# Kernel tuning notes

Hardware: AMD Instinct MI355X
Metric: run time of the kernel (lower is better)

The kernel has to match this reference:

```python
import jax, jax.numpy as jnp
import numpy as np

N_LEVELS = 8
N_FEATS = 8            # features per level
BASE_RES = 16
PER_LEVEL_SCALE = 1.2599210739135742
LOG2_HASHMAP = 19
TABLE_PAD = 8192       # padded per-level table rows (>= max level size 6568)
N_POINTS = 262144


def _level_params(l):
    # tcnn: scale = base * s^l - 1 ; res = ceil(scale)+1 ; size = min(2^19, round_up(res^2, 8))
    scale = BASE_RES * (PER_LEVEL_SCALE ** l) - 1.0
    res = int(np.ceil(scale)) + 1
    size = min(1 << LOG2_HASHMAP, ((res * res + 7) // 8) * 8)
    return float(scale), res, size


def hashgrid_encode(x, table):
    """x: [N,2] in [0,1), table: [L, TABLE_PAD, F]. Returns [N, L*F]."""
    outs = []
    for l in range(N_LEVELS):
        scale, res, size = _level_params(l)
        pos = x * jnp.float32(scale) + jnp.float32(0.5)
        pg = jnp.floor(pos)
        frac = pos - pg
        pg = pg.astype(jnp.int32)
        # Smoothstep interpolation weights: t^2 (3 - 2t)
        w = frac * frac * (3.0 - 2.0 * frac)          # [N,2]
        feat = jnp.zeros((x.shape[0], N_FEATS), dtype=table.dtype)
        for dx in (0, 1):
            wx = w[:, 0] if dx else 1.0 - w[:, 0]
            for dy in (0, 1):
                wy = w[:, 1] if dy else 1.0 - w[:, 1]
                # dense grid index (all levels here fit the hashmap), modulo level size as in tcnn
                idx = ((pg[:, 0] + dx) + (pg[:, 1] + dy) * res) % size
                feat = feat + (wx * wy)[:, None] * table[l, idx]  # irregular gather
        outs.append(feat)
    return jnp.concatenate(outs, axis=-1)  # [N, 64]


def mlp(enc, W0, W1, W2, W3):
    h = jax.nn.relu(enc @ W0)
    h = jax.nn.relu(h @ W1)
    h = jax.nn.relu(h @ W2)
    return h @ W3  # linear output activation


def setup_inputs() -> dict:
    key = jax.random.key(0)
    ks = jax.random.split(key, 6)
    x = jax.random.uniform(ks[0], (N_POINTS, 2), dtype=jnp.float32)
    # tcnn initializes grid params ~ uniform(-1e-4, 1e-4); small values
    table = jax.random.normal(ks[1], (N_LEVELS, TABLE_PAD, N_FEATS), dtype=jnp.float32) * 1e-2
    W0 = jax.random.normal(ks[2], (64, 256), dtype=jnp.float32) * (1.0 / np.sqrt(64))
    W1 = jax.random.normal(ks[3], (256, 256), dtype=jnp.float32) * (1.0 / np.sqrt(256))
    W2 = jax.random.normal(ks[4], (256, 256), dtype=jnp.float32) * (1.0 / np.sqrt(256))
    W3 = jax.random.normal(ks[5], (256, 1), dtype=jnp.float32) * (1.0 / np.sqrt(256))
    return {"x": x, "table": table, "W0": W0, "W1": W1, "W2": W2, "W3": W3}


def reference(x, table, W0, W1, W2, W3):
    enc = hashgrid_encode(x, table)
    return mlp(enc, W0, W1, W2, W3)  # [N, 1]
```

## Files before the change

kernel.cpp:

```cpp
#include <hip/hip_runtime.h>
#include <cmath>


#define N_LEVELS 8
#define TABLE_PAD 8192
#define TILE_M 64
#define ACT_STRIDE 264
#define ENC_STRIDE 72

typedef __attribute__((ext_vector_type(8))) short short8;
typedef __attribute__((ext_vector_type(16))) float float16v;

struct LevelParams {
  float scale[N_LEVELS];
  int   res[N_LEVELS];
  int   size[N_LEVELS];
};

__device__ __forceinline__ unsigned short f2bf(float f) {
  unsigned int u = __float_as_uint(f);
  u += 0x7fffu + ((u >> 16) & 1u);
  return (unsigned short)(u >> 16);
}
__device__ __forceinline__ unsigned int pack2bf(float a, float b) {
  a = a > 0.f ? a : 0.f;
  b = b > 0.f ? b : 0.f;
  return (unsigned int)f2bf(a) | ((unsigned int)f2bf(b) << 16);
}

__global__ void pack_weights_kernel(const float* __restrict__ W0,
                                    const float* __restrict__ W1,
                                    const float* __restrict__ W2,
                                    unsigned short* __restrict__ Wp) {
  int tid = blockIdx.x * blockDim.x + threadIdx.x;
  const float* src;
  int base, e;
  if (tid < 16384)        { src = W0; base = 0;     e = tid;         }
  else if (tid < 81920)   { src = W1; base = 16384; e = tid - 16384; }
  else if (tid < 147456)  { src = W2; base = 81920; e = tid - 81920; }
  else return;
  int ki = e & 15;
  int n  = (e >> 4) & 255;
  int kb = e >> 12;
  unsigned int u = __float_as_uint(src[(kb * 16 + ki) * 256 + n]);
  u += 0x7fffu + ((u >> 16) & 1u);
  Wp[base + e] = (unsigned short)(u >> 16);
}

__global__ __launch_bounds__(512, 6) void neural_field_kernel(
    const float* __restrict__ x,
    const float* __restrict__ table,
    const unsigned short* __restrict__ Wp,
    const float* __restrict__ W3,
    float* __restrict__ out,
    LevelParams P) {
  __shared__ unsigned short bufE[TILE_M * ENC_STRIDE];
  __shared__ unsigned short bufA[TILE_M * ACT_STRIDE];

  const int t  = threadIdx.x;
  const int g0 = blockIdx.x * TILE_M;

  const int lane  = t & 63;
  const int w     = t >> 6;
  const int l31   = lane & 31;
  const int h8    = lane >> 5;
  const int wbase = w * 32;

  const int woff = (wbase + l31) * 16 + h8 * 8;

  {
    int p = t & 63;
    int l = t >> 6;
    float2 xy = ((const float2*)x)[g0 + p];
    float scale = P.scale[l];
    int res = P.res[l], size = P.size[l];
    float posx = xy.x * scale + 0.5f;
    float posy = xy.y * scale + 0.5f;
    float pgx = floorf(posx), pgy = floorf(posy);
    float fx = posx - pgx, fy = posy - pgy;
    float wx = fx * fx * (3.0f - 2.0f * fx);
    float wy = fy * fy * (3.0f - 2.0f * fy);
    int px = (int)pgx, py = (int)pgy;
    float acc[8] = {0, 0, 0, 0, 0, 0, 0, 0};
    for (int dy = 0; dy < 2; ++dy) {
      float wyv = dy ? wy : 1.0f - wy;
      for (int dx = 0; dx < 2; ++dx) {
        float wgt = (dx ? wx : 1.0f - wx) * wyv;
        int idx = (px + dx) + (py + dy) * res;
        if (idx >= size) idx -= size;
        const float4* tp =
            (const float4*)(table + ((size_t)l * TABLE_PAD + idx) * 8);
        float4 t0 = tp[0], t1 = tp[1];
        acc[0] += wgt * t0.x; acc[1] += wgt * t0.y;
        acc[2] += wgt * t0.z; acc[3] += wgt * t0.w;
        acc[4] += wgt * t1.x; acc[5] += wgt * t1.y;
        acc[6] += wgt * t1.z; acc[7] += wgt * t1.w;
      }
    }
    union { unsigned short s[8]; short8 v; } u;
    for (int j = 0; j < 8; ++j) u.s[j] = f2bf(acc[j]);
    *(short8*)&bufE[p * ENC_STRIDE + l * 8] = u.v;
  }

  auto run_layer = [&](const unsigned short* inb, int in_stride,
                       unsigned short* outb, const unsigned short* Wpl,
                       int KB, short8 wf0, bool inplace, bool fuse_final,
                       float* fsum) {
    float16v acc[2];
    for (int j = 0; j < 16; ++j) { acc[0][j] = 0.f; acc[1][j] = 0.f; }

    const unsigned short* ap0 = &inb[l31 * in_stride + h8 * 8];
    const unsigned short* ap1 = ap0 + 32 * in_stride;
    const unsigned short* wp  = Wpl + woff;

    float w3f[16];
    if (fuse_final) {
      for (int q = 0; q < 4; ++q) {
        float4 wv = *(const float4*)(W3 + wbase + 8 * q + 4 * h8);
        w3f[4 * q + 0] = wv.x; w3f[4 * q + 1] = wv.y;
        w3f[4 * q + 2] = wv.z; w3f[4 * q + 3] = wv.w;
      }
    }

    short8 af0[2];
    af0[0] = *(const short8*)(ap0);
    af0[1] = *(const short8*)(ap1);

#pragma unroll
    for (int kb = 0; kb < KB; ++kb) {
      short8 wf1, af1[2];
      int kn = (kb + 1 < KB) ? kb + 1 : kb;
      wf1    = *(const short8*)(wp + kn * 4096);
      af1[0] = *(const short8*)(ap0 + kn * 16);
      af1[1] = *(const short8*)(ap1 + kn * 16);

      acc[0] = __builtin_amdgcn_mfma_f32_32x32x16_bf16(wf0, af0[0], acc[0],
                                                       0, 0, 0);
      acc[1] = __builtin_amdgcn_mfma_f32_32x32x16_bf16(wf0, af0[1], acc[1],
                                                       0, 0, 0);
      wf0 = wf1; af0[0] = af1[0]; af0[1] = af1[1];
    }

    if (inplace) __syncthreads();

    if (!fuse_final) {
      for (int pt = 0; pt < 2; ++pt) {
        int m = pt * 32 + l31;
        for (int q = 0; q < 4; ++q) {
          int n0 = wbase + 8 * q + 4 * h8;
          uint2 pk;
          pk.x = pack2bf(acc[pt][4 * q + 0], acc[pt][4 * q + 1]);
          pk.y = pack2bf(acc[pt][4 * q + 2], acc[pt][4 * q + 3]);
          *(uint2*)&outb[m * ACT_STRIDE + n0] = pk;
        }
      }
    } else {
      float part0 = 0.f, part1 = 0.f;
      for (int j = 0; j < 16; ++j) {
        float v0 = acc[0][j]; v0 = v0 > 0.f ? v0 : 0.f;
        float v1 = acc[1][j]; v1 = v1 > 0.f ? v1 : 0.f;
        part0 += v0 * w3f[j];
        part1 += v1 * w3f[j];
      }
      part0 += __shfl_xor(part0, 32);
      part1 += __shfl_xor(part1, 32);
      float val = h8 ? part1 : part0;
      fsum[lane * 9 + w] = val;
    }
  };

  float* fsum = (float*)bufE;

  short8 wf = *(const short8*)(Wp + woff);
  __syncthreads();
  run_layer(bufE, ENC_STRIDE, bufA, Wp, 4, wf, false, false, fsum);
  wf = *(const short8*)(Wp + 16384 + woff);
  __syncthreads();
  run_layer(bufA, ACT_STRIDE, bufA, Wp + 16384, 16, wf, true, false, fsum);
  wf = *(const short8*)(Wp + 81920 + woff);
  __syncthreads();
  run_layer(bufA, ACT_STRIDE, nullptr, Wp + 81920, 16, wf, false, true, fsum);
  __syncthreads();

  {
    int p = t >> 3;
    int q = t & 7;
    float v = fsum[p * 9 + q];
    v += __shfl_xor(v, 1);
    v += __shfl_xor(v, 2);
    v += __shfl_xor(v, 4);
    if (q == 0) out[g0 + p] = v;
  }
}

extern "C" void kernel_launch(void* const* d_in, const int* in_sizes, int n_in,
                              void* d_out, int out_size, void* d_ws,
                              size_t ws_size, hipStream_t stream) {
  const float* x     = (const float*)d_in[0];
  const float* table = (const float*)d_in[1];
  const float* W0    = (const float*)d_in[2];
  const float* W1    = (const float*)d_in[3];
  const float* W2    = (const float*)d_in[4];
  const float* W3    = (const float*)d_in[5];
  float* out = (float*)d_out;
  int N = in_sizes[0] / 2;

  unsigned short* Wp = (unsigned short*)d_ws;

  LevelParams P;
  const double c = 1.2599210739135742;
  double m = 1.0;
  for (int l = 0; l < N_LEVELS; ++l) {
    double scale_d = 16.0 * m - 1.0;
    int res = (int)std::ceil(scale_d) + 1;
    long long sz = ((long long)res * res + 7) / 8 * 8;
    if (sz > (1LL << 19)) sz = 1LL << 19;
    P.scale[l] = (float)scale_d;
    P.res[l]   = res;
    P.size[l]  = (int)sz;
    m *= c;
  }

  hipLaunchKernelGGL(pack_weights_kernel, dim3(576), dim3(256), 0, stream,
                     W0, W1, W2, Wp);
  hipLaunchKernelGGL(neural_field_kernel, dim3(N / TILE_M), dim3(512), 0,
                     stream, x, table, Wp, W3, out, P);
}
```

Baseline: 156.2 us.

## Enlarge point tile to 96 rows with three MFMA row-tiles per wave

```diff
diff --git a/kernel.cpp b/kernel.cpp
--- a/kernel.cpp
+++ b/kernel.cpp
@@ -4,7 +4,7 @@
 
 #define N_LEVELS 8
 #define TABLE_PAD 8192
-#define TILE_M 64
+#define TILE_M 96
 #define ACT_STRIDE 264
 #define ENC_STRIDE 72
 
@@ -47,13 +47,13 @@
   Wp[base + e] = (unsigned short)(u >> 16);
 }
 
-__global__ __launch_bounds__(512, 6) void neural_field_kernel(
+__global__ __launch_bounds__(512, 4) void neural_field_kernel(
     const float* __restrict__ x,
     const float* __restrict__ table,
     const unsigned short* __restrict__ Wp,
     const float* __restrict__ W3,
     float* __restrict__ out,
-    LevelParams P) {
+    LevelParams P, int Ntot) {
   __shared__ unsigned short bufE[TILE_M * ENC_STRIDE];
   __shared__ unsigned short bufA[TILE_M * ACT_STRIDE];
 
@@ -69,103 +69,115 @@
   const int woff = (wbase + l31) * 16 + h8 * 8;
 
   {
-    int p = t & 63;
-    int l = t >> 6;
-    float2 xy = ((const float2*)x)[g0 + p];
-    float scale = P.scale[l];
-    int res = P.res[l], size = P.size[l];
-    float posx = xy.x * scale + 0.5f;
-    float posy = xy.y * scale + 0.5f;
-    float pgx = floorf(posx), pgy = floorf(posy);
-    float fx = posx - pgx, fy = posy - pgy;
-    float wx = fx * fx * (3.0f - 2.0f * fx);
-    float wy = fy * fy * (3.0f - 2.0f * fy);
-    int px = (int)pgx, py = (int)pgy;
-    float acc[8] = {0, 0, 0, 0, 0, 0, 0, 0};
-    for (int dy = 0; dy < 2; ++dy) {
-      float wyv = dy ? wy : 1.0f - wy;
-      for (int dx = 0; dx < 2; ++dx) {
-        float wgt = (dx ? wx : 1.0f - wx) * wyv;
-        int idx = (px + dx) + (py + dy) * res;
-        if (idx >= size) idx -= size;
-        const float4* tp =
-            (const float4*)(table + ((size_t)l * TABLE_PAD + idx) * 8);
-        float4 t0 = tp[0], t1 = tp[1];
-        acc[0] += wgt * t0.x; acc[1] += wgt * t0.y;
-        acc[2] += wgt * t0.z; acc[3] += wgt * t0.w;
-        acc[4] += wgt * t1.x; acc[5] += wgt * t1.y;
-        acc[6] += wgt * t1.z; acc[7] += wgt * t1.w;
-      }
-    }
-    union { unsigned short s[8]; short8 v; } u;
-    for (int j = 0; j < 8; ++j) u.s[j] = f2bf(acc[j]);
-    *(short8*)&bufE[p * ENC_STRIDE + l * 8] = u.v;
+    int p  = t & 127;
+    int lg = t >> 7;
+    if (p < TILE_M) {
+      int gi = g0 + p;
+      if (gi >= Ntot) gi = Ntot - 1;
+      float2 xy = ((const float2*)x)[gi];
+      for (int li = 0; li < 2; ++li) {
+        int l = lg * 2 + li;
+        float scale = P.scale[l];
+        int res = P.res[l], size = P.size[l];
+        float posx = xy.x * scale + 0.5f;
+        float posy = xy.y * scale + 0.5f;
+        float pgx = floorf(posx), pgy = floorf(posy);
+        float fx = posx - pgx, fy = posy - pgy;
+        float wx = fx * fx * (3.0f - 2.0f * fx);
+        float wy = fy * fy * (3.0f - 2.0f * fy);
+        int px = (int)pgx, py = (int)pgy;
+        float acc[8] = {0, 0, 0, 0, 0, 0, 0, 0};
+        for (int dy = 0; dy < 2; ++dy) {
+          float wyv = dy ? wy : 1.0f - wy;
+          for (int dx = 0; dx < 2; ++dx) {
+            float wgt = (dx ? wx : 1.0f - wx) * wyv;
+            int idx = (px + dx) + (py + dy) * res;
+            if (idx >= size) idx -= size;
+            const float4* tp =
+                (const float4*)(table + ((size_t)l * TABLE_PAD + idx) * 8);
+            float4 t0 = tp[0], t1 = tp[1];
+            acc[0] += wgt * t0.x; acc[1] += wgt * t0.y;
+            acc[2] += wgt * t0.z; acc[3] += wgt * t0.w;
+            acc[4] += wgt * t1.x; acc[5] += wgt * t1.y;
+            acc[6] += wgt * t1.z; acc[7] += wgt * t1.w;
+          }
+        }
+        union { unsigned short s[8]; short8 v; } u;
+        for (int j = 0; j < 8; ++j) u.s[j] = f2bf(acc[j]);
+        *(short8*)&bufE[p * ENC_STRIDE + l * 8] = u.v;
+      }
+    }
   }
 
   auto run_layer = [&](const unsigned short* inb, int in_stride,
                        unsigned short* outb, const unsigned short* Wpl,
                        int KB, short8 wf0, bool inplace, bool fuse_final,
                        float* fsum) {
-    float16v acc[2];
-    for (int j = 0; j < 16; ++j) { acc[0][j] = 0.f; acc[1][j] = 0.f; }
-
-    const unsigned short* ap0 = &inb[l31 * in_stride + h8 * 8];
-    const unsigned short* ap1 = ap0 + 32 * in_stride;
-    const unsigned short* wp  = Wpl + woff;
-
-    float w3f[16];
-    if (fuse_final) {
-      for (int q = 0; q < 4; ++q) {
-        float4 wv = *(const float4*)(W3 + wbase + 8 * q + 4 * h8);
-        w3f[4 * q + 0] = wv.x; w3f[4 * q + 1] = wv.y;
-        w3f[4 * q + 2] = wv.z; w3f[4 * q + 3] = wv.w;
-      }
-    }
-
-    short8 af0[2];
-    af0[0] = *(const short8*)(ap0);
-    af0[1] = *(const short8*)(ap1);
+    float16v acc[3];
+    for (int pt = 0; pt < 3; ++pt)
+      for (int j = 0; j < 16; ++j) acc[pt][j] = 0.f;
+
+    const unsigned short* ap[3];
+    for (int pt = 0; pt < 3; ++pt)
+      ap[pt] = &inb[(pt * 32 + l31) * in_stride + h8 * 8];
+    const unsigned short* wp = Wpl + woff;
+
+    short8 af0[3];
+    for (int pt = 0; pt < 3; ++pt)
+      af0[pt] = *(const short8*)(ap[pt]);
 
 #pragma unroll
     for (int kb = 0; kb < KB; ++kb) {
-      short8 wf1, af1[2];
       int kn = (kb + 1 < KB) ? kb + 1 : kb;
-      wf1    = *(const short8*)(wp + kn * 4096);
-      af1[0] = *(const short8*)(ap0 + kn * 16);
-      af1[1] = *(const short8*)(ap1 + kn * 16);
-
-      acc[0] = __builtin_amdgcn_mfma_f32_32x32x16_bf16(wf0, af0[0], acc[0],
-                                                       0, 0, 0);
-      acc[1] = __builtin_amdgcn_mfma_f32_32x32x16_bf16(wf0, af0[1], acc[1],
-                                                       0, 0, 0);
-      wf0 = wf1; af0[0] = af1[0]; af0[1] = af1[1];
+      short8 wf1 = *(const short8*)(wp + kn * 4096);
+      short8 af1[3];
+      for (int pt = 0; pt < 3; ++pt)
+        af1[pt] = *(const short8*)(ap[pt] + kn * 16);
+
+      for (int pt = 0; pt < 3; ++pt)
+        acc[pt] = __builtin_amdgcn_mfma_f32_32x32x16_bf16(wf0, af0[pt],
+                                                          acc[pt], 0, 0, 0);
+      wf0 = wf1;
+      for (int pt = 0; pt < 3; ++pt) af0[pt] = af1[pt];
     }
 
     if (inplace) __syncthreads();
 
     if (!fuse_final) {
-      for (int pt = 0; pt < 2; ++pt) {
+      for (int pt = 0; pt < 3; ++pt) {
         int m = pt * 32 + l31;
         for (int q = 0; q < 4; ++q) {
           int n0 = wbase + 8 * q + 4 * h8;
           uint2 pk;
           pk.x = pack2bf(acc[pt][4 * q + 0], acc[pt][4 * q + 1]);
           pk.y = pack2bf(acc[pt][4 * q + 2], acc[pt][4 * q + 3]);
-          *(uint2*)&outb[m * ACT_STRIDE + n0] = pk;
+          *(uint2*)&bufA[m * ACT_STRIDE + n0] = pk;
         }
       }
     } else {
-      float part0 = 0.f, part1 = 0.f;
-      for (int j = 0; j < 16; ++j) {
-        float v0 = acc[0][j]; v0 = v0 > 0.f ? v0 : 0.f;
-        float v1 = acc[1][j]; v1 = v1 > 0.f ? v1 : 0.f;
-        part0 += v0 * w3f[j];
-        part1 += v1 * w3f[j];
-      }
-      part0 += __shfl_xor(part0, 32);
-      part1 += __shfl_xor(part1, 32);
-      float val = h8 ? part1 : part0;
-      fsum[lane * 9 + w] = val;
+      float w3f[16];
+      for (int q = 0; q < 4; ++q) {
+        float4 wv = *(const float4*)(W3 + wbase + 8 * q + 4 * h8);
+        w3f[4 * q + 0] = wv.x; w3f[4 * q + 1] = wv.y;
+        w3f[4 * q + 2] = wv.z; w3f[4 * q + 3] = wv.w;
+      }
+      float part[3];
+      for (int pt = 0; pt < 3; ++pt) {
+        float s = 0.f;
+        for (int j = 0; j < 16; ++j) {
+          float v = acc[pt][j]; v = v > 0.f ? v : 0.f;
+          s += v * w3f[j];
+        }
+        part[pt] = s;
+      }
+      for (int pt = 0; pt < 3; ++pt)
+        part[pt] += __shfl_xor(part[pt], 32);
+      if (h8 == 0) {
+        fsum[(l31)      * 9 + w] = part[0];
+        fsum[(32 + l31) * 9 + w] = part[1];
+      } else {
+        fsum[(64 + l31) * 9 + w] = part[2];
+      }
     }
   };
 
@@ -183,13 +195,15 @@
   __syncthreads();
 
   {
-    int p = t >> 3;
-    int q = t & 7;
-    float v = fsum[p * 9 + q];
+    int p = t >> 2;
+    int q = t & 3;
+    float v = fsum[p * 9 + q] + fsum[p * 9 + q + 4];
     v += __shfl_xor(v, 1);
     v += __shfl_xor(v, 2);
-    v += __shfl_xor(v, 4);
-    if (q == 0) out[g0 + p] = v;
+    if (q == 0 && p < TILE_M) {
+      int gi = g0 + p;
+      if (gi < Ntot) out[gi] = v;
+    }
   }
 }
 
@@ -221,8 +235,9 @@
     m *= c;
   }
 
+  int nblocks = (N + TILE_M - 1) / TILE_M;
   hipLaunchKernelGGL(pack_weights_kernel, dim3(576), dim3(256), 0, stream,
                      W0, W1, W2, Wp);
-  hipLaunchKernelGGL(neural_field_kernel, dim3(N / TILE_M), dim3(512), 0,
-                     stream, x, table, Wp, W3, out, P);
-}
+  hipLaunchKernelGGL(neural_field_kernel, dim3(nblocks), dim3(512), 0,
+                     stream, x, table, Wp, W3, out, P, N);
+}
```

Result: no change. 156.9 us (+0.5%).

## Remap MFMA wave tiling to 64 features by 32 points per wave

Applied to the files above, without the earlier changes.

```diff
diff --git a/kernel.cpp b/kernel.cpp
--- a/kernel.cpp
+++ b/kernel.cpp
@@ -1,4 +1,5 @@
 #include <hip/hip_runtime.h>
+#include <hip/hip_bf16.h>
 #include <cmath>
 
 
@@ -22,10 +23,11 @@
   u += 0x7fffu + ((u >> 16) & 1u);
   return (unsigned short)(u >> 16);
 }
-__device__ __forceinline__ unsigned int pack2bf(float a, float b) {
+__device__ __forceinline__ unsigned int pack2bf_relu(float a, float b) {
   a = a > 0.f ? a : 0.f;
   b = b > 0.f ? b : 0.f;
-  return (unsigned int)f2bf(a) | ((unsigned int)f2bf(b) << 16);
+  __hip_bfloat162 h = __float22bfloat162_rn(make_float2(a, b));
+  return *(unsigned int*)&h;
 }
 
 __global__ void pack_weights_kernel(const float* __restrict__ W0,
@@ -64,9 +66,12 @@
   const int w     = t >> 6;
   const int l31   = lane & 31;
   const int h8    = lane >> 5;
-  const int wbase = w * 32;
-
-  const int woff = (wbase + l31) * 16 + h8 * 8;
+  const int fgrp  = w & 3;
+  const int pgrp  = w >> 2;
+  const int fbase = fgrp * 64;
+  const int mrow  = pgrp * 32 + l31;
+
+  const int woff = (fbase + l31) * 16 + h8 * 8;
 
   {
     int p = t & 63;
@@ -103,92 +108,70 @@
   }
 
   auto run_layer = [&](const unsigned short* inb, int in_stride,
-                       unsigned short* outb, const unsigned short* Wpl,
-                       int KB, short8 wf0, bool inplace, bool fuse_final,
-                       float* fsum) {
+                       const unsigned short* Wpl, int KB,
+                       bool inplace, bool fuse_final, float* fsum) {
     float16v acc[2];
     for (int j = 0; j < 16; ++j) { acc[0][j] = 0.f; acc[1][j] = 0.f; }
 
-    const unsigned short* ap0 = &inb[l31 * in_stride + h8 * 8];
-    const unsigned short* ap1 = ap0 + 32 * in_stride;
-    const unsigned short* wp  = Wpl + woff;
-
-    float w3f[16];
-    if (fuse_final) {
-      for (int q = 0; q < 4; ++q) {
-        float4 wv = *(const float4*)(W3 + wbase + 8 * q + 4 * h8);
-        w3f[4 * q + 0] = wv.x; w3f[4 * q + 1] = wv.y;
-        w3f[4 * q + 2] = wv.z; w3f[4 * q + 3] = wv.w;
-      }
-    }
-
-    short8 af0[2];
-    af0[0] = *(const short8*)(ap0);
-    af0[1] = *(const short8*)(ap1);
+    const unsigned short* ap = &inb[mrow * in_stride + h8 * 8];
+    const unsigned short* wp = Wpl + woff;
 
 #pragma unroll
     for (int kb = 0; kb < KB; ++kb) {
-      short8 wf1, af1[2];
-      int kn = (kb + 1 < KB) ? kb + 1 : kb;
-      wf1    = *(const short8*)(wp + kn * 4096);
-      af1[0] = *(const short8*)(ap0 + kn * 16);
-      af1[1] = *(const short8*)(ap1 + kn * 16);
-
-      acc[0] = __builtin_amdgcn_mfma_f32_32x32x16_bf16(wf0, af0[0], acc[0],
+      short8 wf0 = *(const short8*)(wp + kb * 4096);
+      short8 wf1 = *(const short8*)(wp + kb * 4096 + 512);
+      short8 af  = *(const short8*)(ap + kb * 16);
+      acc[0] = __builtin_amdgcn_mfma_f32_32x32x16_bf16(wf0, af, acc[0],
                                                        0, 0, 0);
-      acc[1] = __builtin_amdgcn_mfma_f32_32x32x16_bf16(wf0, af0[1], acc[1],
+      acc[1] = __builtin_amdgcn_mfma_f32_32x32x16_bf16(wf1, af, acc[1],
                                                        0, 0, 0);
-      wf0 = wf1; af0[0] = af1[0]; af0[1] = af1[1];
     }
 
     if (inplace) __syncthreads();
 
     if (!fuse_final) {
-      for (int pt = 0; pt < 2; ++pt) {
-        int m = pt * 32 + l31;
+      for (int f2 = 0; f2 < 2; ++f2) {
         for (int q = 0; q < 4; ++q) {
-          int n0 = wbase + 8 * q + 4 * h8;
+          int n0 = fbase + f2 * 32 + 8 * q + 4 * h8;
           uint2 pk;
-          pk.x = pack2bf(acc[pt][4 * q + 0], acc[pt][4 * q + 1]);
-          pk.y = pack2bf(acc[pt][4 * q + 2], acc[pt][4 * q + 3]);
-          *(uint2*)&outb[m * ACT_STRIDE + n0] = pk;
+          pk.x = pack2bf_relu(acc[f2][4 * q + 0], acc[f2][4 * q + 1]);
+          pk.y = pack2bf_relu(acc[f2][4 * q + 2], acc[f2][4 * q + 3]);
+          *(uint2*)&bufA[mrow * ACT_STRIDE + n0] = pk;
         }
       }
     } else {
-      float part0 = 0.f, part1 = 0.f;
-      for (int j = 0; j < 16; ++j) {
-        float v0 = acc[0][j]; v0 = v0 > 0.f ? v0 : 0.f;
-        float v1 = acc[1][j]; v1 = v1 > 0.f ? v1 : 0.f;
-        part0 += v0 * w3f[j];
-        part1 += v1 * w3f[j];
+      float s = 0.f;
+      for (int f2 = 0; f2 < 2; ++f2) {
+        for (int q = 0; q < 4; ++q) {
+          float4 wv = *(const float4*)(W3 + fbase + f2 * 32 + 8 * q + 4 * h8);
+          float v0 = acc[f2][4 * q + 0]; v0 = v0 > 0.f ? v0 : 0.f;
+          float v1 = acc[f2][4 * q + 1]; v1 = v1 > 0.f ? v1 : 0.f;
+          float v2 = acc[f2][4 * q + 2]; v2 = v2 > 0.f ? v2 : 0.f;
+          float v3 = acc[f2][4 * q + 3]; v3 = v3 > 0.f ? v3 : 0.f;
+          s += v0 * wv.x + v1 * wv.y + v2 * wv.z + v3 * wv.w;
+        }
       }
-      part0 += __shfl_xor(part0, 32);
-      part1 += __shfl_xor(part1, 32);
-      float val = h8 ? part1 : part0;
-      fsum[lane * 9 + w] = val;
+      s += __shfl_xor(s, 32);
+      if (h8 == 0) fsum[mrow * 5 + fgrp] = s;
     }
   };
 
   float* fsum = (float*)bufE;
 
-  short8 wf = *(const short8*)(Wp + woff);
-  __syncthreads();
-  run_layer(bufE, ENC_STRIDE, bufA, Wp, 4, wf, false, false, fsum);
-  wf = *(const short8*)(Wp + 16384 + woff);
-  __syncthreads();
-  run_layer(bufA, ACT_STRIDE, bufA, Wp + 16384, 16, wf, true, false, fsum);
-  wf = *(const short8*)(Wp + 81920 + woff);
-  __syncthreads();
-  run_layer(bufA, ACT_STRIDE, nullptr, Wp + 81920, 16, wf, false, true, fsum);
-  __syncthreads();
-
-  {
-    int p = t >> 3;
-    int q = t & 7;
-    float v = fsum[p * 9 + q];
+  __syncthreads();
+  run_layer(bufE, ENC_STRIDE, Wp,         4,  false, false, fsum);
+  __syncthreads();
+  run_layer(bufA, ACT_STRIDE, Wp + 16384, 16, true,  false, fsum);
+  __syncthreads();
+  run_layer(bufA, ACT_STRIDE, Wp + 81920, 16, false, true,  fsum);
+  __syncthreads();
+
+  if (t < 256) {
+    int p = t >> 2;
+    int q = t & 3;
+    float v = fsum[p * 5 + q];
     v += __shfl_xor(v, 1);
     v += __shfl_xor(v, 2);
-    v += __shfl_xor(v, 4);
     if (q == 0) out[g0 + p] = v;
   }
 }
```

New measurement: 181.3 us. 1.16x slower.
